# Kernel optimization log

Measured on AMD Instinct MI355X. Metric: run time of the kernel, lower is better.

The kernel has to match this reference:

```python
import jax, jax.numpy as jnp
import numpy as np

B, S, H, DK, DV, D = 1024, 8, 16, 32, 32, 512


def setup_inputs() -> dict:
    key = jax.random.key(0)
    ks = jax.random.split(key, 12)
    s = 1.0 / np.sqrt(D)
    return {
        "Q": jax.random.normal(ks[0], (B, S, D), jnp.float32),
        "K": jax.random.normal(ks[1], (B, S, D), jnp.float32),
        "V": jax.random.normal(ks[2], (B, S, D), jnp.float32),
        "attn_mask": jax.random.bernoulli(ks[3], 0.2, (B, S, S)),
        "hyper": jax.random.normal(ks[4], (B, H * S * DK), jnp.float32),
        "Wq": jax.random.normal(ks[5], (H * DK, D), jnp.float32) * s,
        "bq": jnp.zeros((H * DK,), jnp.float32),
        "Wk": jax.random.normal(ks[6], (H * DK, D), jnp.float32) * s,
        "bk": jnp.zeros((H * DK,), jnp.float32),
        "Wv": jax.random.normal(ks[7], (H * DV, D), jnp.float32) * s,
        "bv": jnp.zeros((H * DV,), jnp.float32),
        "Wo": jax.random.normal(ks[8], (D, H * DV), jnp.float32) * s,
        "bo": jnp.zeros((D,), jnp.float32),
        "ln_g": jnp.ones((D,), jnp.float32),
        "ln_b": jnp.zeros((D,), jnp.float32),
    }


def reference(Q, K, V, attn_mask, hyper, Wq, bq, Wk, bk, Wv, bv, Wo, bo, ln_g, ln_b):
    # QKV projections -> [B, H, S, dk]
    q = (Q @ Wq.T + bq).reshape(B, S, H, DK).transpose(0, 2, 1, 3)
    k = (K @ Wk.T + bk).reshape(B, S, H, DK).transpose(0, 2, 1, 3)
    v = (V @ Wv.T + bv).reshape(B, S, H, DV).transpose(0, 2, 1, 3)
    # scaled dot-product attention with mask
    scores = jnp.einsum('bhqd,bhkd->bhqk', q, k) / np.sqrt(DK).astype(np.float32)
    scores = jnp.where(attn_mask[:, None, :, :], -1e9, scores)
    weights = jax.nn.softmax(scores, axis=-1)
    # hyper-gated AV
    context = jnp.einsum('bhqk,bhkd->bhqd', weights, v) * hyper.reshape(B, H, S, DK)
    context = context.transpose(0, 2, 1, 3).reshape(B, S, H * DV)
    # output projection + residual layernorm (eps=1e-5)
    out = context @ Wo.T + bo + Q
    mu = out.mean(axis=-1, keepdims=True)
    var = out.var(axis=-1, keepdims=True)
    out = (out - mu) * jax.lax.rsqrt(var + 1e-5) * ln_g + ln_b
    return (out, weights)
```

## Files before the change

kernel.cpp:

```cpp
#include <hip/hip_runtime.h>
#include <hip/hip_bf16.h>
#include <cstdint>

#define NB 1024
#define ND 512
#define NM 8192

typedef __attribute__((ext_vector_type(8))) short short8;
typedef __attribute__((ext_vector_type(8))) __bf16 bf16x8;
typedef __attribute__((ext_vector_type(4))) float f32x4;
typedef __attribute__((ext_vector_type(4))) unsigned short ushort4v;

__device__ __forceinline__ unsigned short f2bf(float f) {
  uint32_t x = __builtin_bit_cast(uint32_t, f);
  x += 0x7fffu + ((x >> 16) & 1u);
  return (unsigned short)(x >> 16);
}
__device__ __forceinline__ float bf2f(unsigned short u) {
  return __builtin_bit_cast(float, (uint32_t)u << 16);
}
__device__ __forceinline__ f32x4 mfma16(short8 a, short8 b, f32x4 c) {
  return __builtin_amdgcn_mfma_f32_16x16x32_bf16(
      __builtin_bit_cast(bf16x8, a), __builtin_bit_cast(bf16x8, b), c, 0, 0, 0);
}
__device__ __forceinline__ void gl_lds16(const unsigned short* g, unsigned short* lds) {
  __builtin_amdgcn_global_load_lds(
      (const __attribute__((address_space(1))) unsigned int*)g,
      (__attribute__((address_space(3))) unsigned int*)lds, 16, 0, 0);
}

__global__ __launch_bounds__(256) void convert_kernel(
    const float* __restrict__ Q, const float* __restrict__ K, const float* __restrict__ V,
    const float* __restrict__ Wq, const float* __restrict__ Wk, const float* __restrict__ Wv,
    const float* __restrict__ Wo,
    unsigned short* __restrict__ Qb, unsigned short* __restrict__ Kb,
    unsigned short* __restrict__ Vb, unsigned short* __restrict__ Wqb,
    unsigned short* __restrict__ Wkb, unsigned short* __restrict__ Wvb,
    unsigned short* __restrict__ Wob) {
  const int idx = blockIdx.x * 256 + threadIdx.x;
  const float* src;
  unsigned short* dst;
  int off;
  if (idx < 3 * 524288) {
    const int sel = idx >> 19, o = idx & 524287;
    src = sel == 0 ? Q : sel == 1 ? K : V;
    dst = sel == 0 ? Qb : sel == 1 ? Kb : Vb;
    off = o * 8;
  } else {
    const int w = idx - 3 * 524288;
    const int sel = w >> 15, o = w & 32767;
    src = sel == 0 ? Wq : sel == 1 ? Wk : sel == 2 ? Wv : Wo;
    dst = sel == 0 ? Wqb : sel == 1 ? Wkb : sel == 2 ? Wvb : Wob;
    off = o * 8;
  }
  const float4 a = ((const float4*)(src + off))[0];
  const float4 b = ((const float4*)(src + off))[1];
  short8 r;
  r[0] = (short)f2bf(a.x); r[1] = (short)f2bf(a.y);
  r[2] = (short)f2bf(a.z); r[3] = (short)f2bf(a.w);
  r[4] = (short)f2bf(b.x); r[5] = (short)f2bf(b.y);
  r[6] = (short)f2bf(b.z); r[7] = (short)f2bf(b.w);
  *(short8*)(dst + off) = r;
}

template <int MODE>
__device__ __forceinline__ void gemm_tile(const unsigned short* __restrict__ A,
                                          const unsigned short* __restrict__ W,
                                          const float* __restrict__ bias,
                                          const float* __restrict__ resid,
                                          void* __restrict__ C, int mBase, int nBase) {
  __shared__ unsigned short As[128 * 64];
  __shared__ unsigned short Bs[128 * 64];
  const int tid = threadIdx.x;
  const int lane = tid & 63, wid = tid >> 6;
  const int wm = wid >> 2, wn = wid & 3;
  const int l15 = lane & 15, l4 = lane >> 4;
  const int srow = wid * 16;
  const int lrow = lane >> 3, lcol = (lane & 7) * 8;
  f32x4 acc[4][2] = {};

  for (int kt = 0; kt < 8; ++kt) {
    const int kBase = kt * 64;
#pragma unroll
    for (int i = 0; i < 2; ++i) {
      const int r0 = srow + i * 8;
      gl_lds16(A + (size_t)(mBase + r0 + lrow) * ND + kBase + lcol, &As[r0 * 64]);
      gl_lds16(W + (size_t)(nBase + r0 + lrow) * ND + kBase + lcol, &Bs[r0 * 64]);
    }
    __syncthreads();
#pragma unroll
    for (int kk = 0; kk < 2; ++kk) {
      short8 af[4], bf4[2];
#pragma unroll
      for (int m = 0; m < 4; ++m)
        af[m] = *(const short8*)&As[(wm * 64 + m * 16 + l15) * 64 + kk * 32 + l4 * 8];
#pragma unroll
      for (int n = 0; n < 2; ++n)
        bf4[n] = *(const short8*)&Bs[(wn * 32 + n * 16 + l15) * 64 + kk * 32 + l4 * 8];
#pragma unroll
      for (int m = 0; m < 4; ++m)
#pragma unroll
        for (int n = 0; n < 2; ++n)
          acc[m][n] = mfma16(af[m], bf4[n], acc[m][n]);
    }
    __syncthreads();
  }

#pragma unroll
  for (int m = 0; m < 4; ++m)
#pragma unroll
    for (int n = 0; n < 2; ++n) {
      const int gn = nBase + wn * 32 + n * 16 + l15;
      const float bb = bias ? bias[gn] : 0.f;
#pragma unroll
      for (int r4 = 0; r4 < 4; ++r4) {
        const int gm = mBase + wm * 64 + m * 16 + l4 * 4 + r4;
        float val = acc[m][n][r4] + bb;
        if (MODE == 0) {
          ((unsigned short*)C)[(size_t)gm * ND + gn] = f2bf(val);
        } else {
          val += resid[(size_t)gm * ND + gn];
          ((float*)C)[(size_t)gm * ND + gn] = val;
        }
      }
    }
}

__global__ __launch_bounds__(512) void gemm_qkv(
    const unsigned short* __restrict__ Qb, const unsigned short* __restrict__ Kb,
    const unsigned short* __restrict__ Vb, const unsigned short* __restrict__ Wqb,
    const unsigned short* __restrict__ Wkb, const unsigned short* __restrict__ Wvb,
    const float* __restrict__ bq, const float* __restrict__ bk,
    const float* __restrict__ bv, unsigned short* __restrict__ qo,
    unsigned short* __restrict__ ko, unsigned short* __restrict__ vo) {
  const int bid = blockIdx.x;
  const int lid = (bid & 7) * 96 + (bid >> 3);
  const int by = lid / 12, bx = lid % 12;
  const int seg = bx >> 2, nloc = bx & 3;
  const unsigned short* A = seg == 0 ? Qb : seg == 1 ? Kb : Vb;
  const unsigned short* W = seg == 0 ? Wqb : seg == 1 ? Wkb : Wvb;
  const float* bias = seg == 0 ? bq : seg == 1 ? bk : bv;
  unsigned short* C = seg == 0 ? qo : seg == 1 ? ko : vo;
  gemm_tile<0>(A, W, bias, nullptr, C, by * 128, nloc * 128);
}

__global__ __launch_bounds__(512) void gemm_wo(const unsigned short* __restrict__ ctx,
                                               const unsigned short* __restrict__ Wob,
                                               const float* __restrict__ bo,
                                               const float* __restrict__ Qres,
                                               float* __restrict__ out) {
  const int bid = blockIdx.x;
  const int lid = (bid & 7) * 32 + (bid >> 3);
  const int by = lid >> 2, bx = lid & 3;
  gemm_tile<1>(ctx, Wob, bo, Qres, out, by * 128, bx * 128);
}

__global__ __launch_bounds__(256) void attn_kernel(
    const unsigned short* __restrict__ q, const unsigned short* __restrict__ k,
    const unsigned short* __restrict__ v, const int* __restrict__ mask,
    const float* __restrict__ hyper, float* __restrict__ wout,
    unsigned short* __restrict__ ctx) {
  const int tid = threadIdx.x;
  const int wid = tid >> 6, lane = tid & 63;
  const int t = blockIdx.x * 4 + wid;
  const int b = t >> 4, h = t & 15;
  const int i = lane >> 3, j = lane & 7;

  const unsigned short* qrow = q + (size_t)(b * 8 + i) * ND + h * 32;
  const unsigned short* krow = k + (size_t)(b * 8 + j) * ND + h * 32;
  float dot = 0.f;
#pragma unroll
  for (int c = 0; c < 4; ++c) {
    const short8 qv = ((const short8*)qrow)[c];
    const short8 kv = ((const short8*)krow)[c];
#pragma unroll
    for (int e = 0; e < 8; ++e)
      dot += bf2f((unsigned short)qv[e]) * bf2f((unsigned short)kv[e]);
  }
  float score = dot * 0.17677669529663687f;
  if (mask[b * 64 + i * 8 + j]) score = -1e9f;

  float mx = score;
#pragma unroll
  for (int o = 4; o; o >>= 1) mx = fmaxf(mx, __shfl_xor(mx, o, 8));
  const float e = __expf(score - mx);
  float sm = e;
#pragma unroll
  for (int o = 4; o; o >>= 1) sm += __shfl_xor(sm, o, 8);
  const float w = e / sm;
  wout[(size_t)t * 64 + lane] = w;

  const int d0 = (lane & 7) * 4;
  float c0 = 0, c1 = 0, c2 = 0, c3 = 0;
#pragma unroll
  for (int jj = 0; jj < 8; ++jj) {
    const float wj = __shfl(w, jj, 8);
    const ushort4v vv = *(const ushort4v*)(v + (size_t)(b * 8 + jj) * ND + h * 32 + d0);
    c0 += wj * bf2f(vv[0]); c1 += wj * bf2f(vv[1]);
    c2 += wj * bf2f(vv[2]); c3 += wj * bf2f(vv[3]);
  }
  const float4 hv = *(const float4*)(hyper + (size_t)b * 4096 + h * 256 + i * 32 + d0);
  ushort4v co;
  co[0] = f2bf(c0 * hv.x); co[1] = f2bf(c1 * hv.y);
  co[2] = f2bf(c2 * hv.z); co[3] = f2bf(c3 * hv.w);
  *(ushort4v*)(ctx + (size_t)(b * 8 + i) * ND + h * 32 + d0) = co;
}

__global__ __launch_bounds__(256) void ln_kernel(float* __restrict__ io,
                                                 const float* __restrict__ g,
                                                 const float* __restrict__ be) {
  const int tid = threadIdx.x, wid = tid >> 6, lane = tid & 63;
  const size_t row = (size_t)blockIdx.x * 4 + wid;
  float* prow = io + row * ND + lane * 8;
  float4 x0 = ((float4*)prow)[0], x1 = ((float4*)prow)[1];
  float s = x0.x + x0.y + x0.z + x0.w + x1.x + x1.y + x1.z + x1.w;
  float sq = x0.x * x0.x + x0.y * x0.y + x0.z * x0.z + x0.w * x0.w +
             x1.x * x1.x + x1.y * x1.y + x1.z * x1.z + x1.w * x1.w;
#pragma unroll
  for (int o = 32; o; o >>= 1) {
    s += __shfl_xor(s, o, 64);
    sq += __shfl_xor(sq, o, 64);
  }
  const float mu = s * (1.f / 512.f);
  const float inv = rsqrtf(sq * (1.f / 512.f) - mu * mu + 1e-5f);
  const float4 g0 = ((const float4*)(g + lane * 8))[0];
  const float4 g1 = ((const float4*)(g + lane * 8))[1];
  const float4 e0 = ((const float4*)(be + lane * 8))[0];
  const float4 e1 = ((const float4*)(be + lane * 8))[1];
  float4 o0, o1;
  o0.x = (x0.x - mu) * inv * g0.x + e0.x; o0.y = (x0.y - mu) * inv * g0.y + e0.y;
  o0.z = (x0.z - mu) * inv * g0.z + e0.z; o0.w = (x0.w - mu) * inv * g0.w + e0.w;
  o1.x = (x1.x - mu) * inv * g1.x + e1.x; o1.y = (x1.y - mu) * inv * g1.y + e1.y;
  o1.z = (x1.z - mu) * inv * g1.z + e1.z; o1.w = (x1.w - mu) * inv * g1.w + e1.w;
  ((float4*)prow)[0] = o0;
  ((float4*)prow)[1] = o1;
}

extern "C" void kernel_launch(void* const* d_in, const int* in_sizes, int n_in,
                              void* d_out, int out_size, void* d_ws, size_t ws_size,
                              hipStream_t stream) {
  const float* Q = (const float*)d_in[0];
  const float* K = (const float*)d_in[1];
  const float* V = (const float*)d_in[2];
  const int* msk = (const int*)d_in[3];
  const float* hyper = (const float*)d_in[4];
  const float* Wq = (const float*)d_in[5];
  const float* bq = (const float*)d_in[6];
  const float* Wk = (const float*)d_in[7];
  const float* bk = (const float*)d_in[8];
  const float* Wv = (const float*)d_in[9];
  const float* bv = (const float*)d_in[10];
  const float* Wo = (const float*)d_in[11];
  const float* bo = (const float*)d_in[12];
  const float* lg = (const float*)d_in[13];
  const float* lb = (const float*)d_in[14];

  float* out = (float*)d_out;
  float* wout = out + (size_t)NM * ND;

  const size_t MAT = (size_t)NM * ND;
  unsigned short* Qb = (unsigned short*)d_ws;
  unsigned short* Kb = Qb + MAT;
  unsigned short* Vb = Kb + MAT;
  unsigned short* qb = Vb + MAT;
  unsigned short* kb = qb + MAT;
  unsigned short* vb = kb + MAT;
  unsigned short* ctxb = vb + MAT;
  unsigned short* Wqb = ctxb + MAT;
  unsigned short* Wkb = Wqb + (size_t)ND * ND;
  unsigned short* Wvb = Wkb + (size_t)ND * ND;
  unsigned short* Wob = Wvb + (size_t)ND * ND;

  convert_kernel<<<6656, 256, 0, stream>>>(Q, K, V, Wq, Wk, Wv, Wo,
                                           Qb, Kb, Vb, Wqb, Wkb, Wvb, Wob);
  gemm_qkv<<<768, 512, 0, stream>>>(Qb, Kb, Vb, Wqb, Wkb, Wvb,
                                    bq, bk, bv, qb, kb, vb);
  attn_kernel<<<4096, 256, 0, stream>>>(qb, kb, vb, msk, hyper, wout, ctxb);
  gemm_wo<<<256, 512, 0, stream>>>(ctxb, Wob, bo, Q, out);
  ln_kernel<<<2048, 256, 0, stream>>>(out, lg, lb);
}
```

Baseline: 84.14 us.

## Fuse fp32-to-bf16 activation conversion into QKV GEMM loads with swizzled LDS

Drops the separate conversion pass over Q, K and V and instead loads fp32 activations straight inside the QKV GEMM tile loader, converting them to bf16 in registers before writing to LDS. The async global-to-LDS loads are replaced by register-staged loads that write an XOR-swizzled LDS layout, which is meant to avoid bank conflicts on the fragment reads. This removes a full read and write of three 8192x512 activation matrices. In exchange, the GEMM now reads fp32 data (twice the bytes per tile) and each K tile is loaded by every N-tile block, so the conversion work is repeated four times per activation.

Result: faster. 74.64 us (-11.3%).

```diff
diff --git a/kernel.cpp b/kernel.cpp
--- a/kernel.cpp
+++ b/kernel.cpp
@@ -23,48 +23,28 @@
   return __builtin_amdgcn_mfma_f32_16x16x32_bf16(
       __builtin_bit_cast(bf16x8, a), __builtin_bit_cast(bf16x8, b), c, 0, 0, 0);
 }
-__device__ __forceinline__ void gl_lds16(const unsigned short* g, unsigned short* lds) {
-  __builtin_amdgcn_global_load_lds(
-      (const __attribute__((address_space(1))) unsigned int*)g,
-      (__attribute__((address_space(3))) unsigned int*)lds, 16, 0, 0);
-}
-
-__global__ __launch_bounds__(256) void convert_kernel(
-    const float* __restrict__ Q, const float* __restrict__ K, const float* __restrict__ V,
-    const float* __restrict__ Wq, const float* __restrict__ Wk, const float* __restrict__ Wv,
-    const float* __restrict__ Wo,
-    unsigned short* __restrict__ Qb, unsigned short* __restrict__ Kb,
-    unsigned short* __restrict__ Vb, unsigned short* __restrict__ Wqb,
-    unsigned short* __restrict__ Wkb, unsigned short* __restrict__ Wvb,
-    unsigned short* __restrict__ Wob) {
+
+__global__ __launch_bounds__(256) void convert_w(
+    const float* __restrict__ Wq, const float* __restrict__ Wk,
+    const float* __restrict__ Wv, const float* __restrict__ Wo,
+    unsigned short* __restrict__ Wqb, unsigned short* __restrict__ Wkb,
+    unsigned short* __restrict__ Wvb, unsigned short* __restrict__ Wob) {
   const int idx = blockIdx.x * 256 + threadIdx.x;
-  const float* src;
-  unsigned short* dst;
-  int off;
-  if (idx < 3 * 524288) {
-    const int sel = idx >> 19, o = idx & 524287;
-    src = sel == 0 ? Q : sel == 1 ? K : V;
-    dst = sel == 0 ? Qb : sel == 1 ? Kb : Vb;
-    off = o * 8;
-  } else {
-    const int w = idx - 3 * 524288;
-    const int sel = w >> 15, o = w & 32767;
-    src = sel == 0 ? Wq : sel == 1 ? Wk : sel == 2 ? Wv : Wo;
-    dst = sel == 0 ? Wqb : sel == 1 ? Wkb : sel == 2 ? Wvb : Wob;
-    off = o * 8;
-  }
-  const float4 a = ((const float4*)(src + off))[0];
-  const float4 b = ((const float4*)(src + off))[1];
+  const int sel = idx >> 15, o = (idx & 32767) * 8;
+  const float* src = sel == 0 ? Wq : sel == 1 ? Wk : sel == 2 ? Wv : Wo;
+  unsigned short* dst = sel == 0 ? Wqb : sel == 1 ? Wkb : sel == 2 ? Wvb : Wob;
+  const float4 a = ((const float4*)(src + o))[0];
+  const float4 b = ((const float4*)(src + o))[1];
   short8 r;
   r[0] = (short)f2bf(a.x); r[1] = (short)f2bf(a.y);
   r[2] = (short)f2bf(a.z); r[3] = (short)f2bf(a.w);
   r[4] = (short)f2bf(b.x); r[5] = (short)f2bf(b.y);
   r[6] = (short)f2bf(b.z); r[7] = (short)f2bf(b.w);
-  *(short8*)(dst + off) = r;
-}
-
-template <int MODE>
-__device__ __forceinline__ void gemm_tile(const unsigned short* __restrict__ A,
+  *(short8*)(dst + o) = r;
+}
+
+template <bool A_F32, int MODE>
+__device__ __forceinline__ void gemm_tile(const void* __restrict__ A,
                                           const unsigned short* __restrict__ W,
                                           const float* __restrict__ bias,
                                           const float* __restrict__ resid,
@@ -75,28 +55,49 @@
   const int lane = tid & 63, wid = tid >> 6;
   const int wm = wid >> 2, wn = wid & 3;
   const int l15 = lane & 15, l4 = lane >> 4;
-  const int srow = wid * 16;
-  const int lrow = lane >> 3, lcol = (lane & 7) * 8;
   f32x4 acc[4][2] = {};
 
   for (int kt = 0; kt < 8; ++kt) {
     const int kBase = kt * 64;
 #pragma unroll
     for (int i = 0; i < 2; ++i) {
-      const int r0 = srow + i * 8;
-      gl_lds16(A + (size_t)(mBase + r0 + lrow) * ND + kBase + lcol, &As[r0 * 64]);
-      gl_lds16(W + (size_t)(nBase + r0 + lrow) * ND + kBase + lcol, &Bs[r0 * 64]);
+      const int Lb = i * 8192 + tid * 16;
+      const int r = Lb >> 7;
+      const int ce = (Lb & 127) >> 1;
+      const int P = Lb ^ ((r & 7) << 4);
+      short8 av;
+      if (A_F32) {
+        const float* src = (const float*)A + (size_t)(mBase + r) * ND + kBase + ce;
+        const float4 a = ((const float4*)src)[0];
+        const float4 b = ((const float4*)src)[1];
+        av[0] = (short)f2bf(a.x); av[1] = (short)f2bf(a.y);
+        av[2] = (short)f2bf(a.z); av[3] = (short)f2bf(a.w);
+        av[4] = (short)f2bf(b.x); av[5] = (short)f2bf(b.y);
+        av[6] = (short)f2bf(b.z); av[7] = (short)f2bf(b.w);
+      } else {
+        av = *(const short8*)((const unsigned short*)A +
+                              (size_t)(mBase + r) * ND + kBase + ce);
+      }
+      const short8 wv = *(const short8*)(W + (size_t)(nBase + r) * ND + kBase + ce);
+      *(short8*)((char*)As + P) = av;
+      *(short8*)((char*)Bs + P) = wv;
     }
     __syncthreads();
 #pragma unroll
     for (int kk = 0; kk < 2; ++kk) {
       short8 af[4], bf4[2];
 #pragma unroll
-      for (int m = 0; m < 4; ++m)
-        af[m] = *(const short8*)&As[(wm * 64 + m * 16 + l15) * 64 + kk * 32 + l4 * 8];
-#pragma unroll
-      for (int n = 0; n < 2; ++n)
-        bf4[n] = *(const short8*)&Bs[(wn * 32 + n * 16 + l15) * 64 + kk * 32 + l4 * 8];
+      for (int m = 0; m < 4; ++m) {
+        const int r = wm * 64 + m * 16 + l15;
+        const int Lb = r * 128 + kk * 64 + l4 * 16;
+        af[m] = *(const short8*)((char*)As + (Lb ^ ((r & 7) << 4)));
+      }
+#pragma unroll
+      for (int n = 0; n < 2; ++n) {
+        const int r = wn * 32 + n * 16 + l15;
+        const int Lb = r * 128 + kk * 64 + l4 * 16;
+        bf4[n] = *(const short8*)((char*)Bs + (Lb ^ ((r & 7) << 4)));
+      }
 #pragma unroll
       for (int m = 0; m < 4; ++m)
 #pragma unroll
@@ -127,8 +128,8 @@
 }
 
 __global__ __launch_bounds__(512) void gemm_qkv(
-    const unsigned short* __restrict__ Qb, const unsigned short* __restrict__ Kb,
-    const unsigned short* __restrict__ Vb, const unsigned short* __restrict__ Wqb,
+    const float* __restrict__ Q, const float* __restrict__ K,
+    const float* __restrict__ V, const unsigned short* __restrict__ Wqb,
     const unsigned short* __restrict__ Wkb, const unsigned short* __restrict__ Wvb,
     const float* __restrict__ bq, const float* __restrict__ bk,
     const float* __restrict__ bv, unsigned short* __restrict__ qo,
@@ -137,11 +138,11 @@
   const int lid = (bid & 7) * 96 + (bid >> 3);
   const int by = lid / 12, bx = lid % 12;
   const int seg = bx >> 2, nloc = bx & 3;
-  const unsigned short* A = seg == 0 ? Qb : seg == 1 ? Kb : Vb;
+  const float* A = seg == 0 ? Q : seg == 1 ? K : V;
   const unsigned short* W = seg == 0 ? Wqb : seg == 1 ? Wkb : Wvb;
   const float* bias = seg == 0 ? bq : seg == 1 ? bk : bv;
   unsigned short* C = seg == 0 ? qo : seg == 1 ? ko : vo;
-  gemm_tile<0>(A, W, bias, nullptr, C, by * 128, nloc * 128);
+  gemm_tile<true, 0>(A, W, bias, nullptr, C, by * 128, nloc * 128);
 }
 
 __global__ __launch_bounds__(512) void gemm_wo(const unsigned short* __restrict__ ctx,
@@ -152,7 +153,7 @@
   const int bid = blockIdx.x;
   const int lid = (bid & 7) * 32 + (bid >> 3);
   const int by = lid >> 2, bx = lid & 3;
-  gemm_tile<1>(ctx, Wob, bo, Qres, out, by * 128, bx * 128);
+  gemm_tile<false, 1>(ctx, Wob, bo, Qres, out, by * 128, bx * 128);
 }
 
 __global__ __launch_bounds__(256) void attn_kernel(
@@ -259,10 +260,7 @@
   float* wout = out + (size_t)NM * ND;
 
   const size_t MAT = (size_t)NM * ND;
-  unsigned short* Qb = (unsigned short*)d_ws;
-  unsigned short* Kb = Qb + MAT;
-  unsigned short* Vb = Kb + MAT;
-  unsigned short* qb = Vb + MAT;
+  unsigned short* qb = (unsigned short*)d_ws;
   unsigned short* kb = qb + MAT;
   unsigned short* vb = kb + MAT;
   unsigned short* ctxb = vb + MAT;
@@ -271,9 +269,8 @@
   unsigned short* Wvb = Wkb + (size_t)ND * ND;
   unsigned short* Wob = Wvb + (size_t)ND * ND;
 
-  convert_kernel<<<6656, 256, 0, stream>>>(Q, K, V, Wq, Wk, Wv, Wo,
-                                           Qb, Kb, Vb, Wqb, Wkb, Wvb, Wob);
-  gemm_qkv<<<768, 512, 0, stream>>>(Qb, Kb, Vb, Wqb, Wkb, Wvb,
+  convert_w<<<512, 256, 0, stream>>>(Wq, Wk, Wv, Wo, Wqb, Wkb, Wvb, Wob);
+  gemm_qkv<<<768, 512, 0, stream>>>(Q, K, V, Wqb, Wkb, Wvb,
                                     bq, bk, bv, qb, kb, vb);
   attn_kernel<<<4096, 256, 0, stream>>>(qb, kb, vb, msk, hyper, wout, ctxb);
   gemm_wo<<<256, 512, 0, stream>>>(ctxb, Wob, bo, Q, out);
```

## Double-buffer GEMM LDS tiles with XOR swizzle and prefetch next k-tile

Applied to the files above, without the earlier changes.

Replaces the single-buffered GEMM mainloop with a two-stage ping-pong. The next k-tile's global-to-LDS loads are issued before computing on the current one, and a single vmcnt wait plus barrier is used per stage. LDS rows are XOR-swizzled at 16-byte granularity to reduce bank conflicts on the MFMA fragment reads. Launch bounds are raised to request two blocks per CU. The cost is double the LDS footprint (64KB per block), which can limit occupancy.

After: 74.36 us. 1.13x faster.

```diff
diff --git a/kernel.cpp b/kernel.cpp
--- a/kernel.cpp
+++ b/kernel.cpp
@@ -28,6 +28,8 @@
       (const __attribute__((address_space(1))) unsigned int*)g,
       (__attribute__((address_space(3))) unsigned int*)lds, 16, 0, 0);
 }
+#define VMCNT0() asm volatile("s_waitcnt vmcnt(0)" ::: "memory")
+#define BAR() __builtin_amdgcn_s_barrier()
 
 __global__ __launch_bounds__(256) void convert_kernel(
     const float* __restrict__ Q, const float* __restrict__ K, const float* __restrict__ V,
@@ -64,46 +66,68 @@
 }
 
 template <int MODE>
-__device__ __forceinline__ void gemm_tile(const unsigned short* __restrict__ A,
-                                          const unsigned short* __restrict__ W,
-                                          const float* __restrict__ bias,
-                                          const float* __restrict__ resid,
-                                          void* __restrict__ C, int mBase, int nBase) {
-  __shared__ unsigned short As[128 * 64];
-  __shared__ unsigned short Bs[128 * 64];
+__device__ __forceinline__ void gemm2p(const unsigned short* __restrict__ A,
+                                       const unsigned short* __restrict__ W,
+                                       const float* __restrict__ bias,
+                                       const float* __restrict__ resid,
+                                       void* __restrict__ C, int mBase, int nBase) {
+  __shared__ unsigned short As0[128 * 64], As1[128 * 64];
+  __shared__ unsigned short Bs0[128 * 64], Bs1[128 * 64];
   const int tid = threadIdx.x;
   const int lane = tid & 63, wid = tid >> 6;
   const int wm = wid >> 2, wn = wid & 3;
   const int l15 = lane & 15, l4 = lane >> 4;
-  const int srow = wid * 16;
-  const int lrow = lane >> 3, lcol = (lane & 7) * 8;
+  const int lrow = lane >> 3, lgrn = lane & 7;
+  const int rA = wid * 16 + lrow;
+  const int rB = wid * 16 + 8 + lrow;
+  const int gA = (lgrn ^ (rA & 7)) * 8;
+  const int gB = (lgrn ^ (rB & 7)) * 8;
+
   f32x4 acc[4][2] = {};
 
-  for (int kt = 0; kt < 8; ++kt) {
+  auto stage = [&](unsigned short* as, unsigned short* bs, int kt) {
     const int kBase = kt * 64;
-#pragma unroll
-    for (int i = 0; i < 2; ++i) {
-      const int r0 = srow + i * 8;
-      gl_lds16(A + (size_t)(mBase + r0 + lrow) * ND + kBase + lcol, &As[r0 * 64]);
-      gl_lds16(W + (size_t)(nBase + r0 + lrow) * ND + kBase + lcol, &Bs[r0 * 64]);
+    gl_lds16(A + (size_t)(mBase + rA) * ND + kBase + gA, as + (wid * 16) * 64);
+    gl_lds16(A + (size_t)(mBase + rB) * ND + kBase + gB, as + (wid * 16 + 8) * 64);
+    gl_lds16(W + (size_t)(nBase + rA) * ND + kBase + gA, bs + (wid * 16) * 64);
+    gl_lds16(W + (size_t)(nBase + rB) * ND + kBase + gB, bs + (wid * 16 + 8) * 64);
+  };
+  auto compute = [&](const unsigned short* as, const unsigned short* bs) {
+#pragma unroll
+    for (int kk = 0; kk < 2; ++kk) {
+      short8 af[4], bfr[2];
+#pragma unroll
+      for (int m = 0; m < 4; ++m) {
+        const int r = wm * 64 + m * 16 + l15;
+        const int G = kk * 4 + l4;
+        af[m] = *(const short8*)((const char*)as + r * 128 + ((G ^ (r & 7)) * 16));
+      }
+#pragma unroll
+      for (int n = 0; n < 2; ++n) {
+        const int r = wn * 32 + n * 16 + l15;
+        const int G = kk * 4 + l4;
+        bfr[n] = *(const short8*)((const char*)bs + r * 128 + ((G ^ (r & 7)) * 16));
+      }
+#pragma unroll
+      for (int m = 0; m < 4; ++m)
+#pragma unroll
+        for (int n = 0; n < 2; ++n)
+          acc[m][n] = mfma16(af[m], bfr[n], acc[m][n]);
     }
-    __syncthreads();
-#pragma unroll
-    for (int kk = 0; kk < 2; ++kk) {
-      short8 af[4], bf4[2];
-#pragma unroll
-      for (int m = 0; m < 4; ++m)
-        af[m] = *(const short8*)&As[(wm * 64 + m * 16 + l15) * 64 + kk * 32 + l4 * 8];
-#pragma unroll
-      for (int n = 0; n < 2; ++n)
-        bf4[n] = *(const short8*)&Bs[(wn * 32 + n * 16 + l15) * 64 + kk * 32 + l4 * 8];
-#pragma unroll
-      for (int m = 0; m < 4; ++m)
-#pragma unroll
-        for (int n = 0; n < 2; ++n)
-          acc[m][n] = mfma16(af[m], bf4[n], acc[m][n]);
-    }
-    __syncthreads();
+  };
+
+  stage(As0, Bs0, 0);
+  VMCNT0();
+  BAR();
+  for (int kt = 0; kt < 8; kt += 2) {
+    stage(As1, Bs1, kt + 1);
+    compute(As0, Bs0);
+    VMCNT0();
+    BAR();
+    if (kt < 6) stage(As0, Bs0, kt + 2);
+    compute(As1, Bs1);
+    VMCNT0();
+    BAR();
   }
 
 #pragma unroll
@@ -126,7 +150,7 @@
     }
 }
 
-__global__ __launch_bounds__(512) void gemm_qkv(
+__global__ __launch_bounds__(512, 2) void gemm_qkv(
     const unsigned short* __restrict__ Qb, const unsigned short* __restrict__ Kb,
     const unsigned short* __restrict__ Vb, const unsigned short* __restrict__ Wqb,
     const unsigned short* __restrict__ Wkb, const unsigned short* __restrict__ Wvb,
@@ -141,18 +165,18 @@
   const unsigned short* W = seg == 0 ? Wqb : seg == 1 ? Wkb : Wvb;
   const float* bias = seg == 0 ? bq : seg == 1 ? bk : bv;
   unsigned short* C = seg == 0 ? qo : seg == 1 ? ko : vo;
-  gemm_tile<0>(A, W, bias, nullptr, C, by * 128, nloc * 128);
-}
-
-__global__ __launch_bounds__(512) void gemm_wo(const unsigned short* __restrict__ ctx,
-                                               const unsigned short* __restrict__ Wob,
-                                               const float* __restrict__ bo,
-                                               const float* __restrict__ Qres,
-                                               float* __restrict__ out) {
+  gemm2p<0>(A, W, bias, nullptr, C, by * 128, nloc * 128);
+}
+
+__global__ __launch_bounds__(512, 2) void gemm_wo(const unsigned short* __restrict__ ctx,
+                                                  const unsigned short* __restrict__ Wob,
+                                                  const float* __restrict__ bo,
+                                                  const float* __restrict__ Qres,
+                                                  float* __restrict__ out) {
   const int bid = blockIdx.x;
   const int lid = (bid & 7) * 32 + (bid >> 3);
   const int by = lid >> 2, bx = lid & 3;
-  gemm_tile<1>(ctx, Wob, bo, Qres, out, by * 128, bx * 128);
+  gemm2p<1>(ctx, Wob, bo, Qres, out, by * 128, bx * 128);
 }
 
 __global__ __launch_bounds__(256) void attn_kernel(
```
